# Kernel optimization log

Hardware: AMD Instinct MI355X
Metric: run time of the kernel (lower is better)

## Reference

```python
import jax, jax.numpy as jnp
import numpy as np

# arch config (matches init_kwargs)
T = 8
G = 16
D = 64
GG = G * G
THR = 0.5            # arch.object_threshold
Z_COS_MATCH_W = 5.0  # arch.z_cos_match_weight
ADJ_W = 1.0
PRES_W = 1.0
POOL_W = 1.0
OBJ_W = 10.0
FLOW_W = 1.0
FULL_OBJ = 200000.0  # arch.full_object_weight
FLOW_END = 100000.0  # arch.flow_cooling_end_step


def setup_inputs() -> dict:
    key = jax.random.key(0)
    k1, k2, k3 = jax.random.split(key, 3)
    B = 128
    return {
        "z_what": jax.random.normal(k1, (T * B, GG, D), dtype=jnp.float32),
        "z_pres_prob": jax.random.uniform(k2, (T * B, GG, 1), dtype=jnp.float32),
        "grid_flow": jax.random.uniform(k3, (T * B, GG, 1), dtype=jnp.float32),
        "global_step": 50000,
    }


def _maxpool3x3(x):
    # x: (N, C, G, G); torch MaxPool2d(3, stride=1, padding=1) pads with -inf
    return jax.lax.reduce_window(
        x, -jnp.inf, jax.lax.max,
        window_dimensions=(1, 1, 3, 3), window_strides=(1, 1, 1, 1),
        padding=[(0, 0), (0, 0), (1, 1), (1, 1)])


def reference(z_what, z_pres_prob, grid_flow, global_step):
    B = z_what.shape[0] // T
    zw = z_what.reshape(T, B, GG, D)
    zp = z_pres_prob.reshape(T, B, GG, 1)

    # ---- z_what_loss_grid_cell: adjacent squared deltas ----
    z_what_loss = jnp.sum((zw[1:] - zw[:-1]) ** 2)

    # ---- z_pres_loss_grid_cell ----
    sim = 1.0 - (zp[2:] - zp[:-2]) ** 2
    deltas = (zp[2:] - zp[1:-1]) ** 2 + (zp[:-2] - zp[1:-1]) ** 2
    z_pres_loss = jnp.sum(sim * deltas)

    # ---- z_what_consistency_pool (cosine_sim branch) ----
    w = jnp.abs(zw) * zp                                    # (T,B,GG,D)
    wi = w.transpose(0, 1, 3, 2).reshape(T * B, D, G, G)
    smoothed = _maxpool3x3(wi).reshape(T, B, D, GG).transpose(0, 1, 3, 2)
    dot = jnp.sum(smoothed[:-1] * w[1:], axis=-1)           # (T-1,B,GG)
    na = jnp.maximum(jnp.sqrt(jnp.sum(smoothed[:-1] ** 2, -1)), 1e-6)
    nb = jnp.maximum(jnp.sqrt(jnp.sum(w[1:] ** 2, -1)), 1e-6)
    cos_pool = dot / (na * nb)
    pw = zp[..., 0]
    pw = (pw[:-1] + pw[1:]) * 0.5                           # (T-1,B,GG)
    z_what_loss_pool = -jnp.sum(cos_pool * pw)

    # ---- z_what_consistency_objects (vectorized over objects) ----
    # For every active cell (t,b,i,j) at time t<T-1, compare its z_what (prior)
    # with z_what at t+1 over the 3x3 circular neighborhood, restricted to
    # neighbor cells whose z_pres > threshold. Loss per object:
    #   -z_cos_match_weight * max(sim) + sum(sim); skipped if no active neighbor.
    zpg = zp.reshape(T, B, G, G)
    zwg = zw.reshape(T, B, G, G, D)
    prior = zwg[:-1]                                        # (T-1,B,G,G,D)
    prior_n = jnp.maximum(jnp.sqrt(jnp.sum(prior ** 2, -1)), 1e-8)
    pres_prior = zpg[:-1] > THR                             # (T-1,B,G,G)
    sum_sim = jnp.zeros(prior.shape[:-1], dtype=prior.dtype)
    max_sim = jnp.full(prior.shape[:-1], -jnp.inf, dtype=prior.dtype)
    has_nb = jnp.zeros(prior.shape[:-1], dtype=bool)
    for di in (-1, 0, 1):
        for dj in (-1, 0, 1):
            nbw = jnp.roll(zwg[1:], (-di, -dj), axis=(2, 3))       # circular
            nbp = jnp.roll(zpg[1:], (-di, -dj), axis=(2, 3)) > THR
            dotn = jnp.sum(prior * nbw, axis=-1)
            nn = jnp.maximum(jnp.sqrt(jnp.sum(nbw ** 2, -1)), 1e-8)
            s = dotn / (prior_n * nn)
            sum_sim = sum_sim + jnp.where(nbp, s, 0.0)
            max_sim = jnp.maximum(max_sim, jnp.where(nbp, s, -jnp.inf))
            has_nb = has_nb | nbp
    valid = pres_prior & has_nb
    contrib = jnp.where(valid, -Z_COS_MATCH_W * max_sim + sum_sim, 0.0)
    z_what_loss_objects = jnp.sum(contrib)
    objects_detected = jnp.sum(pres_prior.astype(jnp.int32))

    # ---- compute_flow_loss ----
    zp_img = z_pres_prob.reshape(-1, 1, G, G)
    zp_max = _maxpool3x3(zp_img).reshape(-1, GG, 1)
    flow = grid_flow.reshape(-1, GG, 1)
    fmask = flow > 0.5
    flow_loss = jnp.sum(jnp.where(fmask, (zp_max - flow) ** 2, 0.0)) \
        + 100.0 * jnp.maximum(0.0, jnp.sum(zp_img) - jnp.sum(flow))

    # ---- total (Space base loss excluded; external submodule) ----
    scale_obj = min(1.0, float(global_step) / FULL_OBJ)
    scale_flow = max(0.0, 1.0 - float(global_step) / FLOW_END)
    loss = (z_what_loss * ADJ_W
            + z_pres_loss * PRES_W
            + z_what_loss_pool * POOL_W
            + z_what_loss_objects * scale_obj * OBJ_W
            + flow_loss * FLOW_W * scale_flow)
    return loss
```

## Files before the change

kernel.cpp:

```cpp
#include <hip/hip_runtime.h>
#include <math.h>

#define TT 8
#define BB 128
#define GG 256
#define DD 64
#define NCH 4
#define CF4 4
#define ST 5


__device__ inline float wred(float v) {
#pragma unroll
    for (int off = 32; off > 0; off >>= 1) v += __shfl_xor(v, off, 64);
    return v;
}
__device__ inline float dot4(float4 a, float4 b) {
    return a.x * b.x + a.y * b.y + a.z * b.z + a.w * b.w;
}
__device__ inline float4 fabs4(float4 a) {
    return make_float4(fabsf(a.x), fabsf(a.y), fabsf(a.z), fabsf(a.w));
}
__device__ inline float4 max4(float4 a, float4 b) {
    return make_float4(fmaxf(a.x, b.x), fmaxf(a.y, b.y), fmaxf(a.z, b.z), fmaxf(a.w, b.w));
}
__device__ inline float4 scale4(float4 a, float s) {
    return make_float4(a.x * s, a.y * s, a.z * s, a.w * s);
}
__device__ inline float4 sub4(float4 a, float4 b) {
    return make_float4(a.x - b.x, a.y - b.y, a.z - b.z, a.w - b.w);
}

__global__ __launch_bounds__(256) void pair_kernel(const float* __restrict__ zw,
                                                   const float* __restrict__ zp,
                                                   const float* __restrict__ flow,
                                                   float* __restrict__ ws) {
    const int pairIdx = blockIdx.x;
    const int t = pairIdx >> 7;
    const int b = pairIdx & (BB - 1);
    const int tid = threadIdx.x;
    const int gi = tid >> 4, gj = tid & 15;

    __shared__ float4 shW[GG * ST];
    __shared__ float4 shB[GG * ST];
    __shared__ float pA[GG], pB[GG], nB[GG];
    __shared__ float bred[8][4];

    const float4* gA = (const float4*)zw + (size_t)(t * BB + b) * 1024;
    const float4* gB = gA + (size_t)BB * 1024;

    const float pAc = zp[(size_t)(t * BB + b) * GG + tid];
    const float pBc = zp[(size_t)((t + 1) * BB + b) * GG + tid];
    pA[tid] = pAc;
    pB[tid] = pBc;

    int nbc[9];
    unsigned inbM = 0;
    {
        int m = 0;
#pragma unroll
        for (int di = -1; di <= 1; di++) {
#pragma unroll
            for (int dj = -1; dj <= 1; dj++) {
                nbc[m] = (((gi + di) & 15) << 4) | ((gj + dj) & 15);
                if (((unsigned)(gi + di) < 16u) && ((unsigned)(gj + dj) < 16u))
                    inbM |= (1u << m);
                m++;
            }
        }
    }
    __syncthreads();

    float zdiff = 0.f, sa = 0.f, sb = 0.f, poolDot = 0.f, poolN = 0.f;
    float dots[9] = {0.f, 0.f, 0.f, 0.f, 0.f, 0.f, 0.f, 0.f, 0.f};

#pragma unroll 1
    for (int c = 0; c < NCH; c++) {
        float4 aA[CF4], aB[CF4];
#pragma unroll
        for (int q = 0; q < CF4; q++) {
            aA[q] = gA[tid * 16 + c * 4 + q];
            aB[q] = gB[tid * 16 + c * 4 + q];
        }
#pragma unroll
        for (int q = 0; q < CF4; q++) {
            float4 d = sub4(aB[q], aA[q]);
            zdiff += dot4(d, d);
            sa += dot4(aA[q], aA[q]);
            sb += dot4(aB[q], aB[q]);
            dots[4] += dot4(aA[q], aB[q]);
            shW[tid * ST + q] = scale4(fabs4(aA[q]), pAc);
            shB[tid * ST + q] = aB[q];
        }
        __syncthreads();

#pragma unroll
        for (int k = 0; k < 9; k++) {
            if (k == 4) continue;
            int base = nbc[k] * ST;
#pragma unroll
            for (int q = 0; q < CF4; q++) dots[k] += dot4(aA[q], shB[base + q]);
        }

        float4 rm[CF4];
#pragma unroll
        for (int q = 0; q < CF4; q++) rm[q] = scale4(fabs4(aA[q]), pAc);
        if (gj > 0) {
            int base = (tid - 1) * ST;
#pragma unroll
            for (int q = 0; q < CF4; q++) rm[q] = max4(rm[q], shW[base + q]);
        }
        if (gj < 15) {
            int base = (tid + 1) * ST;
#pragma unroll
            for (int q = 0; q < CF4; q++) rm[q] = max4(rm[q], shW[base + q]);
        }
        __syncthreads();
#pragma unroll
        for (int q = 0; q < CF4; q++) shB[tid * ST + q] = rm[q];
        __syncthreads();

        float4 sm[CF4];
#pragma unroll
        for (int q = 0; q < CF4; q++) sm[q] = rm[q];
        if (gi > 0) {
            int base = (tid - 16) * ST;
#pragma unroll
            for (int q = 0; q < CF4; q++) sm[q] = max4(sm[q], shB[base + q]);
        }
        if (gi < 15) {
            int base = (tid + 16) * ST;
#pragma unroll
            for (int q = 0; q < CF4; q++) sm[q] = max4(sm[q], shB[base + q]);
        }
#pragma unroll
        for (int q = 0; q < CF4; q++) {
            poolDot += dot4(sm[q], fabs4(aB[q]));
            poolN += dot4(sm[q], sm[q]);
        }
        __syncthreads();
    }

    nB[tid] = sqrtf(sb);
    __syncthreads();

    float prior_n = fmaxf(sqrtf(sa), 1e-8f);
    float sum_sim = 0.f, max_sim = -1e30f;
    bool has = false;
#pragma unroll
    for (int k = 0; k < 9; k++) {
        float nn = fmaxf(nB[nbc[k]], 1e-8f);
        float s = dots[k] / (prior_n * nn);
        if (pB[nbc[k]] > 0.5f) {
            sum_sim += s;
            max_sim = fmaxf(max_sim, s);
            has = true;
        }
    }
    float obj = ((pAc > 0.5f) && has) ? (sum_sim - 5.0f * max_sim) : 0.f;

    float na_pool = fmaxf(sqrtf(poolN), 1e-6f);
    float nb_pool = fmaxf(pBc * sqrtf(sb), 1e-6f);
    float poolc = -(pBc * poolDot) / (na_pool * nb_pool) * 0.5f * (pAc + pBc);

    float mx = pAc;
#pragma unroll
    for (int k = 0; k < 9; k++)
        if (k != 4 && ((inbM >> k) & 1u)) mx = fmaxf(mx, pA[nbc[k]]);
    float f = flow[(size_t)(t * BB + b) * GG + tid];
    float fsq = 0.f;
    if (f > 0.5f) { float d = mx - f; fsq = d * d; }
    float szp = pAc, sflow = f;
    if (t == 6) {
        float mxB = pBc;
#pragma unroll
        for (int k = 0; k < 9; k++)
            if (k != 4 && ((inbM >> k) & 1u)) mxB = fmaxf(mxB, pB[nbc[k]]);
        float f7 = flow[(size_t)(7 * BB + b) * GG + tid];
        if (f7 > 0.5f) { float d = mxB - f7; fsq += d * d; }
        szp += pBc;
        sflow += f7;
    }

    float pres = 0.f;
    if (t <= 5) {
        float pC = zp[(size_t)((t + 2) * BB + b) * GG + tid];
        float s02 = pC - pAc;
        float sim = 1.f - s02 * s02;
        float d2 = pC - pBc, d0 = pAc - pBc;
        pres = sim * (d2 * d2 + d0 * d0);
    }

    float r[7] = {zdiff, pres, poolc, obj, fsq, szp, sflow};
    int w = tid >> 6, lane = tid & 63;
#pragma unroll
    for (int j = 0; j < 7; j++) {
        float rv = wred(r[j]);
        if (lane == 0) bred[j][w] = rv;
    }
    __syncthreads();
    if (tid < 7)
        ws[pairIdx * 8 + tid] = bred[tid][0] + bred[tid][1] + bred[tid][2] + bred[tid][3];
}

__global__ __launch_bounds__(256) void final_kernel(const float* __restrict__ ws,
                                                    const int* __restrict__ gs,
                                                    float* __restrict__ out) {
    const int tid = threadIdx.x;
    __shared__ float bred[7][4];
    float c[7] = {0.f, 0.f, 0.f, 0.f, 0.f, 0.f, 0.f};
    for (int p = tid; p < (TT - 1) * BB; p += 256) {
        const float* r = ws + p * 8;
#pragma unroll
        for (int j = 0; j < 7; j++) c[j] += r[j];
    }
    int w = tid >> 6, lane = tid & 63;
#pragma unroll
    for (int j = 0; j < 7; j++) {
        float rv = wred(c[j]);
        if (lane == 0) bred[j][w] = rv;
    }
    __syncthreads();
    if (tid == 0) {
        float s[7];
#pragma unroll
        for (int j = 0; j < 7; j++) s[j] = bred[j][0] + bred[j][1] + bred[j][2] + bred[j][3];
        float step = (float)gs[0];
        float scale_obj = fminf(1.f, step / 200000.f);
        float scale_flow = fmaxf(0.f, 1.f - step / 100000.f);
        float flow_loss = s[4] + 100.f * fmaxf(0.f, s[5] - s[6]);
        out[0] = s[0]
               + s[1]
               + s[2]
               + s[3] * scale_obj * 10.0f
               + flow_loss * scale_flow;
    }
}

extern "C" void kernel_launch(void* const* d_in, const int* in_sizes, int n_in,
                              void* d_out, int out_size, void* d_ws, size_t ws_size,
                              hipStream_t stream) {
    const float* zw = (const float*)d_in[0];
    const float* zp = (const float*)d_in[1];
    const float* fl = (const float*)d_in[2];
    const int* gs = (const int*)d_in[3];
    float* ws = (float*)d_ws;

    pair_kernel<<<(TT - 1) * BB, 256, 0, stream>>>(zw, zp, fl, ws);
    final_kernel<<<1, 256, 0, stream>>>(ws, gs, (float*)d_out);
}
```

Baseline: 130.6 us.

## Fuse final reduction via last-block atomic and use shuffles for row maxpool

Replaces the separate final reduction kernel with a last-block-done pattern: each block writes its partials, bumps an atomic counter, and the last block performs the global reduction, with a memset to reset the counter. The horizontal 3x3 max-pool pass now uses wavefront shuffles instead of a shared-memory round trip, which removes two barriers and one shared buffer write per chunk. Shared stride drops from 5 to 4 float4 and launch bounds request 4 blocks per CU. The risks are bank conflicts from the unpadded stride, plus an extra memset launch and the fences.

```diff
diff --git a/kernel.cpp b/kernel.cpp
--- a/kernel.cpp
+++ b/kernel.cpp
@@ -7,7 +7,8 @@
 #define DD 64
 #define NCH 4
 #define CF4 4
-#define ST 5
+#define ST 4
+#define NPAIR ((TT - 1) * BB)
 
 
 __device__ inline float wred(float v) {
@@ -30,21 +31,31 @@
 __device__ inline float4 sub4(float4 a, float4 b) {
     return make_float4(a.x - b.x, a.y - b.y, a.z - b.z, a.w - b.w);
 }
-
-__global__ __launch_bounds__(256) void pair_kernel(const float* __restrict__ zw,
-                                                   const float* __restrict__ zp,
-                                                   const float* __restrict__ flow,
-                                                   float* __restrict__ ws) {
+__device__ inline float4 shfl4(float4 v, int src) {
+    return make_float4(__shfl(v.x, src, 64), __shfl(v.y, src, 64),
+                       __shfl(v.z, src, 64), __shfl(v.w, src, 64));
+}
+
+__global__ __launch_bounds__(256, 4) void pair_kernel(const float* __restrict__ zw,
+                                                      const float* __restrict__ zp,
+                                                      const float* __restrict__ flow,
+                                                      float* __restrict__ wsbase,
+                                                      const int* __restrict__ gs,
+                                                      float* __restrict__ out) {
     const int pairIdx = blockIdx.x;
     const int t = pairIdx >> 7;
     const int b = pairIdx & (BB - 1);
     const int tid = threadIdx.x;
     const int gi = tid >> 4, gj = tid & 15;
-
-    __shared__ float4 shW[GG * ST];
+    const int lane = tid & 63;
+
+    __shared__ float4 shR[GG * ST];
     __shared__ float4 shB[GG * ST];
     __shared__ float pA[GG], pB[GG], nB[GG];
     __shared__ float bred[8][4];
+    __shared__ int isLast;
+
+    float* part = wsbase + 16;
 
     const float4* gA = (const float4*)zw + (size_t)(t * BB + b) * 1024;
     const float4* gB = gA + (size_t)BB * 1024;
@@ -89,8 +100,14 @@
             sa += dot4(aA[q], aA[q]);
             sb += dot4(aB[q], aB[q]);
             dots[4] += dot4(aA[q], aB[q]);
-            shW[tid * ST + q] = scale4(fabs4(aA[q]), pAc);
+            float4 wa = scale4(fabs4(aA[q]), pAc);
+            float4 rm = wa;
+            float4 lft = shfl4(wa, lane - 1);
+            if (gj > 0) rm = max4(rm, lft);
+            float4 rgt = shfl4(wa, lane + 1);
+            if (gj < 15) rm = max4(rm, rgt);
             shB[tid * ST + q] = aB[q];
+            shR[tid * ST + q] = rm;
         }
         __syncthreads();
 
@@ -102,41 +119,13 @@
             for (int q = 0; q < CF4; q++) dots[k] += dot4(aA[q], shB[base + q]);
         }
 
-        float4 rm[CF4];
-#pragma unroll
-        for (int q = 0; q < CF4; q++) rm[q] = scale4(fabs4(aA[q]), pAc);
-        if (gj > 0) {
-            int base = (tid - 1) * ST;
-#pragma unroll
-            for (int q = 0; q < CF4; q++) rm[q] = max4(rm[q], shW[base + q]);
-        }
-        if (gj < 15) {
-            int base = (tid + 1) * ST;
-#pragma unroll
-            for (int q = 0; q < CF4; q++) rm[q] = max4(rm[q], shW[base + q]);
-        }
-        __syncthreads();
-#pragma unroll
-        for (int q = 0; q < CF4; q++) shB[tid * ST + q] = rm[q];
-        __syncthreads();
-
-        float4 sm[CF4];
-#pragma unroll
-        for (int q = 0; q < CF4; q++) sm[q] = rm[q];
-        if (gi > 0) {
-            int base = (tid - 16) * ST;
-#pragma unroll
-            for (int q = 0; q < CF4; q++) sm[q] = max4(sm[q], shB[base + q]);
-        }
-        if (gi < 15) {
-            int base = (tid + 16) * ST;
-#pragma unroll
-            for (int q = 0; q < CF4; q++) sm[q] = max4(sm[q], shB[base + q]);
-        }
 #pragma unroll
         for (int q = 0; q < CF4; q++) {
-            poolDot += dot4(sm[q], fabs4(aB[q]));
-            poolN += dot4(sm[q], sm[q]);
+            float4 sm = shR[tid * ST + q];
+            if (gi > 0) sm = max4(sm, shR[(tid - 16) * ST + q]);
+            if (gi < 15) sm = max4(sm, shR[(tid + 16) * ST + q]);
+            poolDot += dot4(sm, fabs4(aB[q]));
+            poolN += dot4(sm, sm);
         }
         __syncthreads();
     }
@@ -192,7 +181,7 @@
     }
 
     float r[7] = {zdiff, pres, poolc, obj, fsq, szp, sflow};
-    int w = tid >> 6, lane = tid & 63;
+    int w = tid >> 6;
 #pragma unroll
     for (int j = 0; j < 7; j++) {
         float rv = wred(r[j]);
@@ -200,24 +189,26 @@
     }
     __syncthreads();
     if (tid < 7)
-        ws[pairIdx * 8 + tid] = bred[tid][0] + bred[tid][1] + bred[tid][2] + bred[tid][3];
-}
-
-__global__ __launch_bounds__(256) void final_kernel(const float* __restrict__ ws,
-                                                    const int* __restrict__ gs,
-                                                    float* __restrict__ out) {
-    const int tid = threadIdx.x;
-    __shared__ float bred[7][4];
-    float c[7] = {0.f, 0.f, 0.f, 0.f, 0.f, 0.f, 0.f};
-    for (int p = tid; p < (TT - 1) * BB; p += 256) {
-        const float* r = ws + p * 8;
-#pragma unroll
-        for (int j = 0; j < 7; j++) c[j] += r[j];
-    }
-    int w = tid >> 6, lane = tid & 63;
+        part[pairIdx * 8 + tid] = bred[tid][0] + bred[tid][1] + bred[tid][2] + bred[tid][3];
+
+    __threadfence();
+    if (tid == 0) {
+        unsigned old = atomicAdd((unsigned*)wsbase, 1u);
+        isLast = (old == (unsigned)(NPAIR - 1));
+    }
+    __syncthreads();
+    if (!isLast) return;
+    __threadfence();
+
+    float cacc[7] = {0.f, 0.f, 0.f, 0.f, 0.f, 0.f, 0.f};
+    for (int p = tid; p < NPAIR; p += 256) {
+        const float* rr = part + p * 8;
+#pragma unroll
+        for (int j = 0; j < 7; j++) cacc[j] += rr[j];
+    }
 #pragma unroll
     for (int j = 0; j < 7; j++) {
-        float rv = wred(c[j]);
+        float rv = wred(cacc[j]);
         if (lane == 0) bred[j][w] = rv;
     }
     __syncthreads();
@@ -246,6 +237,6 @@
     const int* gs = (const int*)d_in[3];
     float* ws = (float*)d_ws;
 
-    pair_kernel<<<(TT - 1) * BB, 256, 0, stream>>>(zw, zp, fl, ws);
-    final_kernel<<<1, 256, 0, stream>>>(ws, gs, (float*)d_out);
-}
+    hipMemsetAsync(d_ws, 0, 64, stream);
+    pair_kernel<<<NPAIR, 256, 0, stream>>>(zw, zp, fl, ws, gs, (float*)d_out);
+}
```

Measured after the change: 309.8 us. +137.2%, slower.
